# Kernel optimization log

Hardware: AMD Instinct MI355X
Metric: run time of the kernel (lower is better)

Reference implementation:

```python
import jax, jax.numpy as jnp
import numpy as np

B, NV, HID, TDIM = 1024, 256, 256, 128
NODE_IN = 2 + 4 + TDIM  # coords + pos_enc(4) + time_emb


def _sinusoidal_pos_emb(t, dim):
    # standard SinusoidalPosEmb: cat(sin, cos) of t * exp(-i*log(1e4)/(half-1))
    half = dim // 2
    freqs = jnp.exp(-np.log(10000.0) * jnp.arange(half, dtype=t.dtype) / (half - 1))
    ang = t[:, None] * freqs[None, :]
    return jnp.concatenate([jnp.sin(ang), jnp.cos(ang)], axis=-1)  # [B, dim]


def setup_inputs() -> dict:
    key = jax.random.key(0)
    ks = jax.random.split(key, 10)
    s = lambda fan_in: 1.0 / np.sqrt(fan_in)
    return {
        "x": jax.random.normal(ks[0], (B, NV * 2), dtype=jnp.float32),
        "t": jax.random.uniform(ks[1], (B,), dtype=jnp.float32) * 1000.0,
        "time_w": jax.random.normal(ks[2], (TDIM, TDIM), dtype=jnp.float32) * s(TDIM),
        "time_b": jnp.zeros((TDIM,), dtype=jnp.float32),
        "W0": jax.random.normal(ks[3], (NODE_IN, HID), dtype=jnp.float32) * s(NODE_IN),
        "b0": jnp.zeros((HID,), dtype=jnp.float32),
        "W1": jax.random.normal(ks[4], (HID, HID), dtype=jnp.float32) * s(HID),
        "b1": jnp.zeros((HID,), dtype=jnp.float32),
        "W2": jax.random.normal(ks[5], (HID, HID), dtype=jnp.float32) * s(HID),
        "b2": jnp.zeros((HID,), dtype=jnp.float32),
    }


def reference(x, t, time_w, time_b, W0, b0, W1, b1, W2, b2):
    Bsz, D = x.shape
    n = D // 2
    coords = x.reshape(Bsz, n, 2)  # [B, n, 2]

    # cycle positional features (pos_enc_dim=4): sin/cos of vertex angle + 2nd harmonic
    pos = jnp.arange(n, dtype=x.dtype)
    theta = (2.0 * jnp.pi) * pos / n
    pe = jnp.stack([jnp.sin(theta), jnp.cos(theta), jnp.sin(2.0 * theta), jnp.cos(2.0 * theta)], axis=-1)
    pe = jnp.broadcast_to(pe[None], (Bsz, n, 4))

    # time MLP: SinusoidalPosEmb -> Linear -> SiLU, broadcast to every node of the graph
    temb = jax.nn.silu(_sinusoidal_pos_emb(t, time_w.shape[0]) @ time_w + time_b)  # [B, TDIM]
    temb = jnp.broadcast_to(temb[:, None, :], (Bsz, n, temb.shape[-1]))

    h = jnp.concatenate([coords, pe, temb], axis=-1)  # [B, n, NODE_IN]

    # GCN layers over cycle adjacency with self-loops, symmetric-normalized (deg=3 -> 1/3).
    # Cycle structure: neighbors are prev/next vertex within each polygon -> jnp.roll on axis 1.
    for W, b in ((W0, b0), (W1, b1), (W2, b2)):
        s = h @ W + b  # support = x W + b
        agg = (s + jnp.roll(s, 1, axis=1) + jnp.roll(s, -1, axis=1)) / 3.0
        h = jax.nn.silu(agg)

    # mean pooling per graph (scatter_mean over graph_index == mean over vertex axis here)
    return h.mean(axis=1)  # [B, HID]
```

## Files before the change

### kernel.cpp

```cpp
#include <hip/hip_runtime.h>
#include <cstdint>

typedef __attribute__((ext_vector_type(8)))  short bf16x8;
typedef __attribute__((ext_vector_type(16))) float f32x16;
typedef __attribute__((ext_vector_type(2)))  float f32x2;
typedef __attribute__((ext_vector_type(4)))  int   i32x4;

__device__ __forceinline__ unsigned short f2bf(float x) {
  unsigned u = __float_as_uint(x);
  u += 0x7fffu + ((u >> 16) & 1u);
  return (unsigned short)(u >> 16);
}
__device__ __forceinline__ float bf2f(unsigned short h) {
  return __uint_as_float(((unsigned)h) << 16);
}
__device__ __forceinline__ unsigned pk2bf(float lo, float hi) {
#if defined(__has_builtin)
#if __has_builtin(__builtin_amdgcn_cvt_pk_bf16_f32)
  auto v = __builtin_amdgcn_cvt_pk_bf16_f32(lo, hi);
  unsigned u; __builtin_memcpy(&u, &v, 4); return u;
#else
  return ((unsigned)f2bf(hi) << 16) | (unsigned)f2bf(lo);
#endif
#else
  return ((unsigned)f2bf(hi) << 16) | (unsigned)f2bf(lo);
#endif
}
__device__ __forceinline__ float exp2_f(float x) {
#if defined(__has_builtin)
#if __has_builtin(__builtin_amdgcn_exp2f)
  return __builtin_amdgcn_exp2f(x);
#else
  return __builtin_exp2f(x);
#endif
#else
  return __builtin_exp2f(x);
#endif
}
__device__ __forceinline__ float silu_f(float v) {
  return v * __builtin_amdgcn_rcpf(1.0f + __expf(-v));
}
__device__ __forceinline__ unsigned lo_pack(unsigned x, unsigned y) {
  return __builtin_amdgcn_perm(y, x, 0x05040100u);
}
__device__ __forceinline__ unsigned hi_pack(unsigned x, unsigned y) {
  return __builtin_amdgcn_perm(y, x, 0x07060302u);
}

__global__ void pack_kernel(const float* __restrict__ W0, const float* __restrict__ W1,
                            const float* __restrict__ W2,
                            unsigned short* __restrict__ packW) {
  __shared__ float ldsF[16][257];
  const int s = blockIdx.x, tid = threadIdx.x;
  const float* W; int KT, kmax, base, kt;
  if (s < 9)       { W = W0; KT = 9;  kmax = 134; base = 0;      kt = s; }
  else if (s < 25) { W = W1; KT = 16; kmax = 256; base = 36864;  kt = s - 9; }
  else             { W = W2; KT = 16; kmax = 256; base = 102400; kt = s - 25; }
  const int k0 = kt * 16;
#pragma unroll
  for (int i = 0; i < 8; ++i) {
    const int idx = i * 512 + tid;
    const int kl = idx >> 8, col = idx & 255;
    const int kg = k0 + kl;
    ldsF[kl][col] = (kg < kmax) ? W[kg * 256 + col] : 0.0f;
  }
  __syncthreads();
  const int g = tid >> 7, t = (tid >> 6) & 1, lane = tid & 63;
  const int col = g * 64 + t * 32 + (lane & 31);
  const int kb = 8 * (lane >> 5);
  unsigned u0 = pk2bf(ldsF[kb + 0][col], ldsF[kb + 1][col]);
  unsigned u1 = pk2bf(ldsF[kb + 2][col], ldsF[kb + 3][col]);
  unsigned u2 = pk2bf(ldsF[kb + 4][col], ldsF[kb + 5][col]);
  unsigned u3 = pk2bf(ldsF[kb + 6][col], ldsF[kb + 7][col]);
  unsigned short* dst = packW + base + g * (KT * 1024) + t * (KT * 512) + kt * 512 + lane * 8;
  i32x4 v = { (int)u0, (int)u1, (int)u2, (int)u3 };
  *(i32x4*)dst = v;
}

template <int KT, int LAYER>
__device__ __forceinline__ void gcn_layer(
    const int w, const int lane, const int q, const int c, const int sig,
    const unsigned short* __restrict__ packL,
    const float* __restrict__ BIAS,
    const bf16x8* Aold, bf16x8* Anew,
    unsigned int* bndu, unsigned int* scr3_w, float* poolw) {
  const float T  = 0.33333333333f;
  const float L2E = 1.44269504f;
  const float NL2 = -0.69314718f;

  bf16x8 pf0 = ((const bf16x8*)packL)[lane];
  bf16x8 pf1 = ((const bf16x8*)(packL + KT * 512))[lane];

#pragma unroll
  for (int g = 0; g < 4; ++g) {
    const unsigned short* srcg = packL + g * (KT * 1024);
    f32x16 acc0, acc1;
#pragma unroll
    for (int i = 0; i < 16; ++i) { acc0[i] = 0.f; acc1[i] = 0.f; }
    {
      const bf16x8* wb0 = (const bf16x8*)srcg;
      const bf16x8* wb1 = (const bf16x8*)(srcg + KT * 512);
      acc0 = __builtin_amdgcn_mfma_f32_32x32x16_bf16(Aold[0], pf0, acc0, 0, 0, 0);
      acc1 = __builtin_amdgcn_mfma_f32_32x32x16_bf16(Aold[0], pf1, acc1, 0, 0, 0);
#pragma unroll
      for (int kt = 1; kt < KT; ++kt) {
        bf16x8 b0 = wb0[kt * 64 + lane];
        bf16x8 b1 = wb1[kt * 64 + lane];
        acc0 = __builtin_amdgcn_mfma_f32_32x32x16_bf16(Aold[kt], b0, acc0, 0, 0, 0);
        acc1 = __builtin_amdgcn_mfma_f32_32x32x16_bf16(Aold[kt], b1, acc1, 0, 0, 0);
      }
    }

    if (g < 3) {
      const unsigned short* nxt = packL + (g + 1) * (KT * 1024);
      pf0 = ((const bf16x8*)nxt)[lane];
      pf1 = ((const bf16x8*)(nxt + KT * 512))[lane];
    }

    unsigned int* bndp = bndu + (g & 1) * 1024;
    if (q == 0) bndp[(w * 2 + 0) * 32 + c] = pk2bf(acc0[0],  acc1[0]);
    else        bndp[(w * 2 + 1) * 32 + c] = pk2bf(acc0[15], acc1[15]);
    __syncthreads();

    const float e0t0  = __shfl_xor(acc0[0], 32);
    const float e0t1  = __shfl_xor(acc1[0], 32);
    const float e15t0 = __shfl_xor(acc0[15], 32);
    const float e15t1 = __shfl_xor(acc1[15], 32);
    const unsigned pbu = bndp[(((w + 7) & 7) * 2 + 1) * 32 + c];
    const unsigned nbu = bndp[(((w + 1) & 7) * 2 + 0) * 32 + c];
    const float bp0 = bf2f((unsigned short)(pbu & 0xffff));
    const float bp1 = bf2f((unsigned short)(pbu >> 16));
    const float bn0 = bf2f((unsigned short)(nbu & 0xffff));
    const float bn1 = bf2f((unsigned short)(nbu >> 16));
    const float bias0 = BIAS[g * 64 + c], bias1 = BIAS[g * 64 + 32 + c];
    f32x2 cT2;  cT2.x = -L2E * T;      cT2.y = -L2E * T;
    f32x2 nb2;  nb2.x = -L2E * bias0;  nb2.y = -L2E * bias1;
    f32x2 ps2;  ps2.x = 0.f;           ps2.y = 0.f;
#pragma unroll
    for (int r = 0; r < 16; ++r) {
      f32x2 pr2, nx2, ac2;
      if (r > 0)  { pr2.x = acc0[r - 1]; pr2.y = acc1[r - 1]; }
      else        { pr2.x = q ? e15t0 : bp0; pr2.y = q ? e15t1 : bp1; }
      if (r < 15) { nx2.x = acc0[r + 1]; nx2.y = acc1[r + 1]; }
      else        { nx2.x = q ? bn0 : e0t0; nx2.y = q ? bn1 : e0t1; }
      ac2.x = acc0[r]; ac2.y = acc1[r];
      f32x2 s2 = (pr2 + ac2) + nx2;
      f32x2 n2 = s2 * cT2 + nb2;
      f32x2 v2 = n2 * NL2;
      f32x2 e2; e2.x = exp2_f(n2.x); e2.y = exp2_f(n2.y);
      f32x2 d2 = e2 + 1.0f;
      f32x2 r2; r2.x = __builtin_amdgcn_rcpf(d2.x); r2.y = __builtin_amdgcn_rcpf(d2.y);
      f32x2 y2 = v2 * r2;
      if constexpr (LAYER == 2) { ps2 += y2; }
      else scr3_w[(16 * q + r) * 34 + c] = pk2bf(y2.x, y2.y);
    }

    if constexpr (LAYER == 2) {
      float s0 = ps2.x + __shfl_xor(ps2.x, 32);
      float s1 = ps2.y + __shfl_xor(ps2.y, 32);
      if (q == 0) { poolw[w * 256 + g * 64 + c]      = s0;
                    poolw[w * 256 + g * 64 + 32 + c] = s1; }
    } else {
      const unsigned int* sb = scr3_w + sig * 34;
      uint2 d0 = *(const uint2*)(sb + 8 * q + 0);
      uint2 d1 = *(const uint2*)(sb + 8 * q + 2);
      uint2 d2 = *(const uint2*)(sb + 8 * q + 4);
      uint2 d3 = *(const uint2*)(sb + 8 * q + 6);
      uint2 e0 = *(const uint2*)(sb + 16 + 8 * q + 0);
      uint2 e1 = *(const uint2*)(sb + 16 + 8 * q + 2);
      uint2 e2 = *(const uint2*)(sb + 16 + 8 * q + 4);
      uint2 e3 = *(const uint2*)(sb + 16 + 8 * q + 6);
      i32x4 f0 = { (int)lo_pack(d0.x, d0.y), (int)lo_pack(d1.x, d1.y),
                   (int)lo_pack(d2.x, d2.y), (int)lo_pack(d3.x, d3.y) };
      i32x4 f1 = { (int)lo_pack(e0.x, e0.y), (int)lo_pack(e1.x, e1.y),
                   (int)lo_pack(e2.x, e2.y), (int)lo_pack(e3.x, e3.y) };
      i32x4 f2v = { (int)hi_pack(d0.x, d0.y), (int)hi_pack(d1.x, d1.y),
                    (int)hi_pack(d2.x, d2.y), (int)hi_pack(d3.x, d3.y) };
      i32x4 f3 = { (int)hi_pack(e0.x, e0.y), (int)hi_pack(e1.x, e1.y),
                   (int)hi_pack(e2.x, e2.y), (int)hi_pack(e3.x, e3.y) };
      Anew[g * 4 + 0] = __builtin_bit_cast(bf16x8, f0);
      Anew[g * 4 + 1] = __builtin_bit_cast(bf16x8, f1);
      Anew[g * 4 + 2] = __builtin_bit_cast(bf16x8, f2v);
      Anew[g * 4 + 3] = __builtin_bit_cast(bf16x8, f3);
    }
  }
}

__global__ __launch_bounds__(512, 2) void poly_kernel(
    const float* __restrict__ x, const float* __restrict__ t,
    const float* __restrict__ tw, const float* __restrict__ tb,
    const unsigned short* __restrict__ packW,
    const float* __restrict__ B0, const float* __restrict__ B1,
    const float* __restrict__ B2, float* __restrict__ out) {
  __shared__ __align__(16) unsigned int   bndu[2048];
  __shared__ __align__(16) unsigned int   scr3[8 * 1088];
  __shared__ __align__(16) unsigned short temb_sh[160];

  const int tid = threadIdx.x;
  const int w = tid >> 6, lane = tid & 63;
  const int q = lane >> 5, c = lane & 31;
  const int b = blockIdx.x;
  const int sig = (c & 3) + 4 * ((c >> 3) & 3) + 16 * ((c >> 2) & 1);

  {
    float* e_sh = (float*)bndu;
    float* part = (float*)scr3;
    if (tid < 128) {
      const float tv = t[b];
      const int i = tid & 63;
      const float f = expf(-0.14619588396823767f * (float)i);
      const float ang = tv * f;
      e_sh[tid] = (tid < 64) ? sinf(ang) : cosf(ang);
    }
    __syncthreads();
    {
      const int j = tid & 127, p = tid >> 7;
      float a = 0.f;
#pragma unroll 8
      for (int kk = 0; kk < 32; ++kk) {
        const int k = p * 32 + kk;
        a += e_sh[k] * tw[k * 128 + j];
      }
      part[tid] = a;
    }
    __syncthreads();
    if (tid < 128) {
      const float a = tb[tid] + part[tid] + part[128 + tid] + part[256 + tid] + part[384 + tid];
      temb_sh[6 + tid] = f2bf(silu_f(a));
      if (tid < 6)  temb_sh[tid] = 0;
      if (tid < 10) temb_sh[134 + tid] = 0;
    }
    __syncthreads();
  }

  bf16x8 A0[9], A1[16], A2[16];
  {
#pragma unroll
    for (int kt = 0; kt < 9; ++kt)
      A0[kt] = *(const bf16x8*)(temb_sh + kt * 16 + q * 8);
    if (q == 0) {
      const int n = w * 32 + sig;
      const float2 xy = ((const float2*)x)[b * 256 + n];
      const float th = 0.024543692605870074f * (float)n;
      A0[0][0] = (short)f2bf(xy.x);
      A0[0][1] = (short)f2bf(xy.y);
      A0[0][2] = (short)f2bf(sinf(th));
      A0[0][3] = (short)f2bf(cosf(th));
      A0[0][4] = (short)f2bf(sinf(2.f * th));
      A0[0][5] = (short)f2bf(cosf(2.f * th));
    }
  }

  unsigned int* scr3_w = scr3 + w * 1088;
  float* poolw = (float*)scr3;
  gcn_layer< 9, 0>(w, lane, q, c, sig, packW,          B0, A0, A1, bndu, scr3_w, poolw);
  gcn_layer<16, 1>(w, lane, q, c, sig, packW + 36864,  B1, A1, A2, bndu, scr3_w, poolw);
  gcn_layer<16, 2>(w, lane, q, c, sig, packW + 102400, B2, A2, A1, bndu, scr3_w, poolw);

  __syncthreads();
  if (tid < 256) {
    float s = 0.f;
#pragma unroll
    for (int ww = 0; ww < 8; ++ww) s += poolw[ww * 256 + tid];
    out[b * 256 + tid] = s * (1.f / 256.f);
  }
}

extern "C" void kernel_launch(void* const* d_in, const int* in_sizes, int n_in,
                              void* d_out, int out_size, void* d_ws, size_t ws_size,
                              hipStream_t stream) {
  const float* x  = (const float*)d_in[0];
  const float* t  = (const float*)d_in[1];
  const float* tw = (const float*)d_in[2];
  const float* tb = (const float*)d_in[3];
  const float* W0 = (const float*)d_in[4];
  const float* b0 = (const float*)d_in[5];
  const float* W1 = (const float*)d_in[6];
  const float* b1 = (const float*)d_in[7];
  const float* W2 = (const float*)d_in[8];
  const float* b2 = (const float*)d_in[9];

  unsigned short* packW = (unsigned short*)d_ws;
  float* out = (float*)d_out;

  pack_kernel<<<41, 512, 0, stream>>>(W0, W1, W2, packW);
  poly_kernel<<<1024, 512, 0, stream>>>(x, t, tw, tb, packW, b0, b1, b2, out);
}
```

Baseline: 208.1 us.

## Fold time-embedding contribution of layer 0 into a per-graph effective bias

Layer 0's input has a time-embedding part that is the same for every node of a graph, so its product with W0 becomes a per-graph bias vector, computed once per block with a scalar dot product. The layer-0 MFMA then only covers the 6 coordinate and positional-encoding features, one K-tile instead of nine, and its aggregation and SiLU are inlined. The pack kernel changes to a new layout: a 6-row W0 MFMA tile, a separate bf16 row-major copy of the time rows of W0, and shifted offsets for W1 and W2. The trade is an extra 256x128 scalar dot product per block plus extra LDS, in exchange for removing eight MFMA K-steps over 256 columns on every wave.

New measurement: 205.0 us. No clear change (-1.5%).

```diff
diff --git a/kernel.cpp b/kernel.cpp
--- a/kernel.cpp
+++ b/kernel.cpp
@@ -52,29 +52,52 @@
                             unsigned short* __restrict__ packW) {
   __shared__ float ldsF[16][257];
   const int s = blockIdx.x, tid = threadIdx.x;
-  const float* W; int KT, kmax, base, kt;
-  if (s < 9)       { W = W0; KT = 9;  kmax = 134; base = 0;      kt = s; }
-  else if (s < 25) { W = W1; KT = 16; kmax = 256; base = 36864;  kt = s - 9; }
-  else             { W = W2; KT = 16; kmax = 256; base = 102400; kt = s - 25; }
+  if (s == 0) {
+#pragma unroll
+    for (int i = 0; i < 8; ++i) {
+      const int idx = i * 512 + tid;
+      const int kl = idx >> 8, col = idx & 255;
+      ldsF[kl][col] = (kl < 6) ? W0[kl * 256 + col] : 0.0f;
+    }
+    __syncthreads();
+    {
+      const int j = tid >> 6, lane = tid & 63;
+      const int col = j * 32 + (lane & 31);
+      const int kb = 8 * (lane >> 5);
+      i32x4 v = { (int)pk2bf(ldsF[kb + 0][col], ldsF[kb + 1][col]),
+                  (int)pk2bf(ldsF[kb + 2][col], ldsF[kb + 3][col]),
+                  (int)pk2bf(ldsF[kb + 4][col], ldsF[kb + 5][col]),
+                  (int)pk2bf(ldsF[kb + 6][col], ldsF[kb + 7][col]) };
+      *(i32x4*)(packW + j * 512 + lane * 8) = v;
+    }
+    unsigned short* pw0m = packW + 135168;
+#pragma unroll
+    for (int it = 0; it < 64; ++it) {
+      const int idx = it * 512 + tid;
+      const int k = idx >> 8, col = idx & 255;
+      pw0m[k * 256 + col] = f2bf(W0[(6 + k) * 256 + col]);
+    }
+    return;
+  }
+  const float* W; int base, kt;
+  if (s <= 16) { W = W1; base = 4096;  kt = s - 1; }
+  else         { W = W2; base = 69632; kt = s - 17; }
   const int k0 = kt * 16;
 #pragma unroll
   for (int i = 0; i < 8; ++i) {
     const int idx = i * 512 + tid;
     const int kl = idx >> 8, col = idx & 255;
-    const int kg = k0 + kl;
-    ldsF[kl][col] = (kg < kmax) ? W[kg * 256 + col] : 0.0f;
+    ldsF[kl][col] = W[(k0 + kl) * 256 + col];
   }
   __syncthreads();
   const int g = tid >> 7, t = (tid >> 6) & 1, lane = tid & 63;
   const int col = g * 64 + t * 32 + (lane & 31);
   const int kb = 8 * (lane >> 5);
-  unsigned u0 = pk2bf(ldsF[kb + 0][col], ldsF[kb + 1][col]);
-  unsigned u1 = pk2bf(ldsF[kb + 2][col], ldsF[kb + 3][col]);
-  unsigned u2 = pk2bf(ldsF[kb + 4][col], ldsF[kb + 5][col]);
-  unsigned u3 = pk2bf(ldsF[kb + 6][col], ldsF[kb + 7][col]);
-  unsigned short* dst = packW + base + g * (KT * 1024) + t * (KT * 512) + kt * 512 + lane * 8;
-  i32x4 v = { (int)u0, (int)u1, (int)u2, (int)u3 };
-  *(i32x4*)dst = v;
+  i32x4 v = { (int)pk2bf(ldsF[kb + 0][col], ldsF[kb + 1][col]),
+              (int)pk2bf(ldsF[kb + 2][col], ldsF[kb + 3][col]),
+              (int)pk2bf(ldsF[kb + 4][col], ldsF[kb + 5][col]),
+              (int)pk2bf(ldsF[kb + 6][col], ldsF[kb + 7][col]) };
+  *(i32x4*)(packW + base + g * 16384 + t * 8192 + kt * 512 + lane * 8) = v;
 }
 
 template <int KT, int LAYER>
@@ -110,7 +133,6 @@
         acc1 = __builtin_amdgcn_mfma_f32_32x32x16_bf16(Aold[kt], b1, acc1, 0, 0, 0);
       }
     }
-
     if (g < 3) {
       const unsigned short* nxt = packL + (g + 1) * (KT * 1024);
       pf0 = ((const bf16x8*)nxt)[lane];
@@ -193,8 +215,9 @@
     const float* __restrict__ B0, const float* __restrict__ B1,
     const float* __restrict__ B2, float* __restrict__ out) {
   __shared__ __align__(16) unsigned int   bndu[2048];
+  __shared__ __align__(16) unsigned int   bndL0[2048];
   __shared__ __align__(16) unsigned int   scr3[8 * 1088];
-  __shared__ __align__(16) unsigned short temb_sh[160];
+  __shared__ float biasEff[256];
 
   const int tid = threadIdx.x;
   const int w = tid >> 6, lane = tid & 63;
@@ -203,8 +226,9 @@
   const int sig = (c & 3) + 4 * ((c >> 3) & 3) + 16 * ((c >> 2) & 1);
 
   {
-    float* e_sh = (float*)bndu;
-    float* part = (float*)scr3;
+    float* e_sh   = (float*)bndu;
+    float* part   = (float*)scr3;
+    float* temb_f = (float*)bndL0;
     if (tid < 128) {
       const float tv = t[b];
       const int i = tid & 63;
@@ -226,36 +250,125 @@
     __syncthreads();
     if (tid < 128) {
       const float a = tb[tid] + part[tid] + part[128 + tid] + part[256 + tid] + part[384 + tid];
-      temb_sh[6 + tid] = f2bf(silu_f(a));
-      if (tid < 6)  temb_sh[tid] = 0;
-      if (tid < 10) temb_sh[134 + tid] = 0;
-    }
-    __syncthreads();
-  }
-
-  bf16x8 A0[9], A1[16], A2[16];
+      temb_f[tid] = bf2f(f2bf(silu_f(a)));
+    }
+    __syncthreads();
+    {
+      const unsigned short* pw0m = packW + 135168;
+      const int col = tid & 255, p = tid >> 8;
+      float a = 0.f;
+#pragma unroll 8
+      for (int kk = 0; kk < 64; ++kk) {
+        const int k = p * 64 + kk;
+        a += temb_f[k] * bf2f(pw0m[k * 256 + col]);
+      }
+      part[tid] = a;
+    }
+    __syncthreads();
+    if (tid < 256) biasEff[tid] = B0[tid] + part[tid] + part[256 + tid];
+  }
+
+  bf16x8 A1[16], A2[16];
   {
-#pragma unroll
-    for (int kt = 0; kt < 9; ++kt)
-      A0[kt] = *(const bf16x8*)(temb_sh + kt * 16 + q * 8);
+    bf16x8 A00 = {};
     if (q == 0) {
       const int n = w * 32 + sig;
       const float2 xy = ((const float2*)x)[b * 256 + n];
       const float th = 0.024543692605870074f * (float)n;
-      A0[0][0] = (short)f2bf(xy.x);
-      A0[0][1] = (short)f2bf(xy.y);
-      A0[0][2] = (short)f2bf(sinf(th));
-      A0[0][3] = (short)f2bf(cosf(th));
-      A0[0][4] = (short)f2bf(sinf(2.f * th));
-      A0[0][5] = (short)f2bf(cosf(2.f * th));
+      A00[0] = (short)f2bf(xy.x);
+      A00[1] = (short)f2bf(xy.y);
+      A00[2] = (short)f2bf(sinf(th));
+      A00[3] = (short)f2bf(cosf(th));
+      A00[4] = (short)f2bf(sinf(2.f * th));
+      A00[5] = (short)f2bf(cosf(2.f * th));
+    }
+    f32x16 acc[8];
+#pragma unroll
+    for (int j = 0; j < 8; ++j)
+#pragma unroll
+      for (int i = 0; i < 16; ++i) acc[j][i] = 0.f;
+    {
+      const bf16x8* wb = (const bf16x8*)packW;
+#pragma unroll
+      for (int j = 0; j < 8; ++j) {
+        bf16x8 bf = wb[j * 64 + lane];
+        acc[j] = __builtin_amdgcn_mfma_f32_32x32x16_bf16(A00, bf, acc[j], 0, 0, 0);
+      }
+    }
+    {
+      unsigned int* myb = bndL0 + (w * 2 + q) * 128;
+      const int rr = q ? 15 : 0;
+#pragma unroll
+      for (int cg = 0; cg < 4; ++cg)
+        myb[cg * 32 + c] = pk2bf(acc[2 * cg][rr], acc[2 * cg + 1][rr]);
+    }
+    __syncthreads();
+
+    const float T  = 0.33333333333f;
+    const float L2E = 1.44269504f;
+    const float NL2 = -0.69314718f;
+    unsigned int* scr3_w = scr3 + w * 1088;
+#pragma unroll
+    for (int cg = 0; cg < 4; ++cg) {
+      const int j0 = 2 * cg, j1 = 2 * cg + 1;
+      const float e0t0  = __shfl_xor(acc[j0][0], 32);
+      const float e0t1  = __shfl_xor(acc[j1][0], 32);
+      const float e15t0 = __shfl_xor(acc[j0][15], 32);
+      const float e15t1 = __shfl_xor(acc[j1][15], 32);
+      const unsigned pbu = bndL0[(((w + 7) & 7) * 2 + 1) * 128 + cg * 32 + c];
+      const unsigned nbu = bndL0[(((w + 1) & 7) * 2 + 0) * 128 + cg * 32 + c];
+      const float bp0 = bf2f((unsigned short)(pbu & 0xffff));
+      const float bp1 = bf2f((unsigned short)(pbu >> 16));
+      const float bn0 = bf2f((unsigned short)(nbu & 0xffff));
+      const float bn1 = bf2f((unsigned short)(nbu >> 16));
+      const float bias0 = biasEff[cg * 64 + c], bias1 = biasEff[cg * 64 + 32 + c];
+      f32x2 cT2;  cT2.x = -L2E * T;      cT2.y = -L2E * T;
+      f32x2 nb2;  nb2.x = -L2E * bias0;  nb2.y = -L2E * bias1;
+#pragma unroll
+      for (int r = 0; r < 16; ++r) {
+        f32x2 pr2, nx2, ac2;
+        if (r > 0)  { pr2.x = acc[j0][r - 1]; pr2.y = acc[j1][r - 1]; }
+        else        { pr2.x = q ? e15t0 : bp0; pr2.y = q ? e15t1 : bp1; }
+        if (r < 15) { nx2.x = acc[j0][r + 1]; nx2.y = acc[j1][r + 1]; }
+        else        { nx2.x = q ? bn0 : e0t0; nx2.y = q ? bn1 : e0t1; }
+        ac2.x = acc[j0][r]; ac2.y = acc[j1][r];
+        f32x2 s2 = (pr2 + ac2) + nx2;
+        f32x2 n2 = s2 * cT2 + nb2;
+        f32x2 v2 = n2 * NL2;
+        f32x2 e2; e2.x = exp2_f(n2.x); e2.y = exp2_f(n2.y);
+        f32x2 d2 = e2 + 1.0f;
+        f32x2 r2; r2.x = __builtin_amdgcn_rcpf(d2.x); r2.y = __builtin_amdgcn_rcpf(d2.y);
+        f32x2 y2 = v2 * r2;
+        scr3_w[(16 * q + r) * 34 + c] = pk2bf(y2.x, y2.y);
+      }
+      const unsigned int* sb = scr3_w + sig * 34;
+      uint2 d0 = *(const uint2*)(sb + 8 * q + 0);
+      uint2 d1 = *(const uint2*)(sb + 8 * q + 2);
+      uint2 d2 = *(const uint2*)(sb + 8 * q + 4);
+      uint2 d3 = *(const uint2*)(sb + 8 * q + 6);
+      uint2 e0 = *(const uint2*)(sb + 16 + 8 * q + 0);
+      uint2 e1 = *(const uint2*)(sb + 16 + 8 * q + 2);
+      uint2 e2 = *(const uint2*)(sb + 16 + 8 * q + 4);
+      uint2 e3 = *(const uint2*)(sb + 16 + 8 * q + 6);
+      i32x4 f0 = { (int)lo_pack(d0.x, d0.y), (int)lo_pack(d1.x, d1.y),
+                   (int)lo_pack(d2.x, d2.y), (int)lo_pack(d3.x, d3.y) };
+      i32x4 f1 = { (int)lo_pack(e0.x, e0.y), (int)lo_pack(e1.x, e1.y),
+                   (int)lo_pack(e2.x, e2.y), (int)lo_pack(e3.x, e3.y) };
+      i32x4 f2v = { (int)hi_pack(d0.x, d0.y), (int)hi_pack(d1.x, d1.y),
+                    (int)hi_pack(d2.x, d2.y), (int)hi_pack(d3.x, d3.y) };
+      i32x4 f3 = { (int)hi_pack(e0.x, e0.y), (int)hi_pack(e1.x, e1.y),
+                   (int)hi_pack(e2.x, e2.y), (int)hi_pack(e3.x, e3.y) };
+      A1[cg * 4 + 0] = __builtin_bit_cast(bf16x8, f0);
+      A1[cg * 4 + 1] = __builtin_bit_cast(bf16x8, f1);
+      A1[cg * 4 + 2] = __builtin_bit_cast(bf16x8, f2v);
+      A1[cg * 4 + 3] = __builtin_bit_cast(bf16x8, f3);
     }
   }
 
   unsigned int* scr3_w = scr3 + w * 1088;
   float* poolw = (float*)scr3;
-  gcn_layer< 9, 0>(w, lane, q, c, sig, packW,          B0, A0, A1, bndu, scr3_w, poolw);
-  gcn_layer<16, 1>(w, lane, q, c, sig, packW + 36864,  B1, A1, A2, bndu, scr3_w, poolw);
-  gcn_layer<16, 2>(w, lane, q, c, sig, packW + 102400, B2, A2, A1, bndu, scr3_w, poolw);
+  gcn_layer<16, 1>(w, lane, q, c, sig, packW + 4096,  B1, A1, A2, bndu, scr3_w, poolw);
+  gcn_layer<16, 2>(w, lane, q, c, sig, packW + 69632, B2, A2, A1, bndu, scr3_w, poolw);
 
   __syncthreads();
   if (tid < 256) {
@@ -283,6 +396,6 @@
   unsigned short* packW = (unsigned short*)d_ws;
   float* out = (float*)d_out;
 
-  pack_kernel<<<41, 512, 0, stream>>>(W0, W1, W2, packW);
+  pack_kernel<<<33, 512, 0, stream>>>(W0, W1, W2, packW);
   poly_kernel<<<1024, 512, 0, stream>>>(x, t, tw, tb, packW, b0, b1, b2, out);
 }
```
